# Kernel tuning notes

Hardware: AMD Instinct MI355X
Metric: run time of the kernel (lower is better)

## Reference

```python
import jax, jax.numpy as jnp
import numpy as np

B, L, D, H = 2, 2048, 1024, 16


def setup_inputs() -> dict:
    key = jax.random.key(0)
    ks = jax.random.split(key, 6)
    return {
        "x": jax.random.normal(ks[0], (B, L, D), dtype=jnp.float32),
        "w_qkv": jax.random.normal(ks[1], (3 * D, D), dtype=jnp.float32) * (D ** -0.5),
        "b_qkv": jax.random.normal(ks[2], (3 * D,), dtype=jnp.float32) * 0.02,
        "w_out": jax.random.normal(ks[3], (D, D), dtype=jnp.float32) * (D ** -0.5),
        "b_out": jax.random.normal(ks[4], (D,), dtype=jnp.float32) * 0.02,
        "lam": jnp.float32(0.5),
        "heads": H,
    }


def reference(x, w_qkv, b_qkv, w_out, b_out, lam, heads):
    b, l, d = x.shape
    dh = d // heads
    scale = d ** -0.5  # NOTE: module scales by d_model**-0.5, not head_dim**-0.5

    qkv = x @ w_qkv.T + b_qkv                      # [B, L, 3D]
    qkv = qkv.reshape(b, l, 3, heads, dh)
    qkv = jnp.transpose(qkv, (2, 0, 3, 1, 4))      # [3, B, H, L, dh]
    q, k, v = qkv[0], qkv[1], qkv[2]

    k_prev = jnp.roll(k, shift=1, axis=2)          # roll along sequence dim

    s_cur = jnp.einsum("bhqd,bhkd->bhqk", q, k) * scale
    s_prev = jnp.einsum("bhqd,bhkd->bhqk", q, k_prev) * scale

    a1 = jax.nn.softmax(s_cur, axis=-1)
    a2 = jax.nn.softmax(s_prev, axis=-1)
    diff = lam * (a1 - a2)                         # dropout = identity (eval)

    o = jnp.einsum("bhqk,bhkd->bhqd", diff, v)     # [B, H, L, dh]
    o = jnp.transpose(o, (0, 2, 1, 3)).reshape(b, l, d)
    return o @ w_out.T + b_out
```

## Files before the change

kernel.cpp:

```cpp
#include <hip/hip_runtime.h>
#include <hip/hip_bf16.h>
#include <stdint.h>


typedef __attribute__((ext_vector_type(8))) short s16x8;
typedef __attribute__((ext_vector_type(4))) short s16x4;
typedef __attribute__((ext_vector_type(4))) float f32x4;

__device__ __forceinline__ float bf2f(unsigned short u) {
    union { unsigned int i; float f; } x; x.i = ((unsigned int)u) << 16; return x.f;
}
__device__ __forceinline__ unsigned short f2bf(float f) {
    union { float f; unsigned int i; } x; x.f = f;
    unsigned int r = x.i + 0x7FFFu + ((x.i >> 16) & 1u);
    return (unsigned short)(r >> 16);
}

__device__ __forceinline__ f32x4 mfma16(s16x4 a, s16x4 b, f32x4 c) {
#if __has_builtin(__builtin_amdgcn_mfma_f32_16x16x16bf16_1k)
    return __builtin_amdgcn_mfma_f32_16x16x16bf16_1k(a, b, c, 0, 0, 0);
#else
    f32x4 d;
    asm volatile("v_mfma_f32_16x16x16_bf16 %0, %1, %2, %3\n\ts_nop 7\n\ts_nop 3"
                 : "=v"(d) : "v"(a), "v"(b), "v"(c));
    return d;
#endif
}

__device__ __forceinline__ void gload16(const void* g, void* l) {
    auto gp = reinterpret_cast<const __attribute__((address_space(1))) unsigned int*>(
        reinterpret_cast<uintptr_t>(g));
    auto lp = reinterpret_cast<__attribute__((address_space(3))) unsigned int*>(
        reinterpret_cast<uintptr_t>(l));
    __builtin_amdgcn_global_load_lds(gp, lp, 16, 0, 0);
}

__global__ __launch_bounds__(256) void cvt_all(
    const float* __restrict__ x, const float* __restrict__ wq,
    const float* __restrict__ wo,
    unsigned short* __restrict__ xb, unsigned short* __restrict__ wqb,
    unsigned short* __restrict__ wob)
{
    int i4 = blockIdx.x * 256 + threadIdx.x;
    const float* src; unsigned short* dst; int off;
    if (i4 < 1048576)            { src = x;  dst = xb;  off = i4; }
    else if (i4 < 1048576 + 786432) { src = wq; dst = wqb; off = i4 - 1048576; }
    else                         { src = wo; dst = wob; off = i4 - 1835008; }
    float4 v = ((const float4*)src)[off];
    ushort4 u;
    u.x = f2bf(v.x); u.y = f2bf(v.y); u.z = f2bf(v.z); u.w = f2bf(v.w);
    ((ushort4*)dst)[off] = u;
}

__global__ __launch_bounds__(256) void vd_transpose(
    const unsigned short* __restrict__ qkvb, unsigned short* __restrict__ vdt)
{
    __shared__ unsigned short T[64][72];
    const int tid = threadIdx.x;
    const int j0 = blockIdx.x * 64;
    const int bh = blockIdx.y, b = bh >> 4, h = bh & 15;
    const unsigned short* vb = qkvb + (size_t)b * 2048 * 3072 + 2048 + h * 64;

    int r = tid >> 2, cq = tid & 3;
    int j = j0 + r, jn = (j + 1) & 2047;
    const unsigned short* p0 = vb + (size_t)j  * 3072 + cq * 16;
    const unsigned short* p1 = vb + (size_t)jn * 3072 + cq * 16;
    s16x8 a0 = *(const s16x8*)p0, a1 = *(const s16x8*)(p0 + 8);
    s16x8 b0 = *(const s16x8*)p1, b1 = *(const s16x8*)(p1 + 8);
#pragma unroll
    for (int u = 0; u < 8; ++u)
        T[cq * 16 + u][r] = f2bf(bf2f((unsigned short)a0[u]) - bf2f((unsigned short)b0[u]));
#pragma unroll
    for (int u = 0; u < 8; ++u)
        T[cq * 16 + 8 + u][r] = f2bf(bf2f((unsigned short)a1[u]) - bf2f((unsigned short)b1[u]));
    __syncthreads();

    int row = tid >> 2, sc = tid & 3;
    s16x8 o0 = *(const s16x8*)&T[row][sc * 16];
    s16x8 o1 = *(const s16x8*)&T[row][sc * 16 + 8];
    unsigned short* dst = vdt + ((size_t)bh * 64 + row) * 2048 + j0 + sc * 16;
    *(s16x8*)dst = o0;
    *(s16x8*)(dst + 8) = o1;
}

template <int OUT_BF16, int BN>
__global__ __launch_bounds__(256) void gemm_nt_mfma(
    const unsigned short* __restrict__ A,
    const unsigned short* __restrict__ Bm,
    const float* __restrict__ bias,
    void* __restrict__ C,
    int M, int N, int K, int nscale, float smul)
{
    constexpr int NT = BN / 32;
    __shared__ unsigned short As[2][128][32];
    __shared__ unsigned short Bs[2][BN][32];

    const int tid = threadIdx.x;
    const int wave = tid >> 6, lane = tid & 63;
    const int quad = lane >> 4, ln = lane & 15;
    const int wm = (wave >> 1) * 64, wn = (wave & 1) * (NT * 16);
    const int m0 = blockIdx.y * 128, n0 = blockIdx.x * BN;
    const int rA = wave * 16 + (lane >> 2);
    const int gsl = lane & 3;

    f32x4 acc[4][NT];
#pragma unroll
    for (int mt = 0; mt < 4; ++mt)
#pragma unroll
        for (int nt = 0; nt < NT; ++nt) acc[mt][nt] = f32x4{0.f, 0.f, 0.f, 0.f};

    auto stage = [&](int p, int k0) {
#pragma unroll
        for (int q = 0; q < 2; ++q) {
            int row = q * 64 + rA;
            int kg = gsl ^ ((row >> 1) & 3);
            gload16(A + (size_t)(m0 + row) * K + k0 + kg * 8,
                    &As[p][q * 64 + wave * 16][0]);
            if (q * 64 < BN)
                gload16(Bm + (size_t)(n0 + row) * K + k0 + kg * 8,
                        &Bs[p][q * 64 + wave * 16][0]);
        }
    };

    stage(0, 0);
    __syncthreads();
    int p = 0;
    for (int k0 = 0; k0 < K; k0 += 32) {
        if (k0 + 32 < K) stage(p ^ 1, k0 + 32);
        s16x8 af[4], bfr[NT];
#pragma unroll
        for (int mt = 0; mt < 4; ++mt) {
            int rr = wm + mt * 16 + ln;
            af[mt] = *(const s16x8*)&As[p][rr][((quad ^ ((rr >> 1) & 3)) & 3) * 8];
        }
#pragma unroll
        for (int nt = 0; nt < NT; ++nt) {
            int rr = wn + nt * 16 + ln;
            bfr[nt] = *(const s16x8*)&Bs[p][rr][((quad ^ ((rr >> 1) & 3)) & 3) * 8];
        }
#pragma unroll
        for (int mt = 0; mt < 4; ++mt)
#pragma unroll
            for (int nt = 0; nt < NT; ++nt)
                acc[mt][nt] = __builtin_amdgcn_mfma_f32_16x16x32_bf16(
                    af[mt], bfr[nt], acc[mt][nt], 0, 0, 0);
        __syncthreads();
        p ^= 1;
    }

    float bb[NT];
#pragma unroll
    for (int nt = 0; nt < NT; ++nt) bb[nt] = bias[n0 + wn + nt * 16 + ln];
#pragma unroll
    for (int mt = 0; mt < 4; ++mt)
#pragma unroll
        for (int nt = 0; nt < NT; ++nt) {
            int col = n0 + wn + nt * 16 + ln;
            float sc = (col < nscale) ? smul : 1.f;
#pragma unroll
            for (int rg = 0; rg < 4; ++rg) {
                int row = m0 + wm + mt * 16 + quad * 4 + rg;
                float v = (acc[mt][nt][rg] + bb[nt]) * sc;
                if (OUT_BF16)
                    ((unsigned short*)C)[(size_t)row * N + col] = f2bf(v);
                else
                    ((float*)C)[(size_t)row * N + col] = v;
            }
        }
}

__global__ __launch_bounds__(256) void diff_attn_v5(
    const unsigned short* __restrict__ qkv,
    const unsigned short* __restrict__ vdt,
    const float* __restrict__ lam_p,
    unsigned short* __restrict__ o_ws)
{
    constexpr int L = 2048, TD = 3072;

    __shared__ unsigned short Ks[2][64][64];
    __shared__ unsigned short Vs[2][64][64];

    const int tid = threadIdx.x;
    const int wave = tid >> 6, lane = tid & 63;
    const int quad = lane >> 4, ln = lane & 15;
    const int bh = blockIdx.y, b = bh >> 4, h = bh & 15;
    const int q0 = blockIdx.x * 128;
    const size_t seqbase = (size_t)b * L;
    const unsigned short* base = qkv + seqbase * TD + h * 64;
    const unsigned short* kb = base + 1024;
    const unsigned short* vbase = vdt + (size_t)bh * 64 * 2048;

    const int lsl = lane >> 3;
    const int cgl = (lane & 7) ^ lsl;

    s16x8 qf[2][2];
#pragma unroll
    for (int s = 0; s < 2; ++s) {
        const unsigned short* qrow =
            base + (size_t)(q0 + wave * 32 + s * 16 + ln) * TD;
        qf[s][0] = *(const s16x8*)(qrow + quad * 8);
        qf[s][1] = *(const s16x8*)(qrow + 32 + quad * 8);
    }

    auto stage = [&](int p, int j0) {
        const unsigned short* k0p = kb + (size_t)(j0 + wave * 16 + lsl) * TD + cgl * 8;
        gload16(k0p,                  &Ks[p][wave * 16][0]);
        gload16(k0p + (size_t)8 * TD, &Ks[p][wave * 16 + 8][0]);
        const unsigned short* v0p = vbase + (size_t)(wave * 16 + lsl) * 2048 + j0 + cgl * 8;
        gload16(v0p,            &Vs[p][wave * 16][0]);
        gload16(v0p + 8 * 2048, &Vs[p][wave * 16 + 8][0]);
    };

    f32x4 Ot[2][4];
    f32x4 lacc[2];
#pragma unroll
    for (int s = 0; s < 2; ++s) {
        lacc[s] = f32x4{0.f, 0.f, 0.f, 0.f};
#pragma unroll
        for (int mt = 0; mt < 4; ++mt) Ot[s][mt] = f32x4{0.f, 0.f, 0.f, 0.f};
    }

    const s16x4 ones = {(short)0x3F80, (short)0x3F80, (short)0x3F80, (short)0x3F80};
    const int kx0 = (quad ^ (ln & 7)) << 3;
    const int kx1 = ((quad + 4) ^ (ln & 7)) << 3;

    stage(0, 0);
    __syncthreads();
    int p = 0;
    for (int kt = 0; kt < 32; ++kt) {
        if (kt + 1 < 32) stage(p ^ 1, (kt + 1) * 64);

        f32x4 ST[2][4];
#pragma unroll
        for (int t = 0; t < 4; ++t) {
            s16x8 k0 = *(const s16x8*)&Ks[p][t * 16 + ln][kx0];
            s16x8 k1 = *(const s16x8*)&Ks[p][t * 16 + ln][kx1];
#pragma unroll
            for (int s = 0; s < 2; ++s) {
                f32x4 z = f32x4{0.f, 0.f, 0.f, 0.f};
                z = __builtin_amdgcn_mfma_f32_16x16x32_bf16(k0, qf[s][0], z, 0, 0, 0);
                z = __builtin_amdgcn_mfma_f32_16x16x32_bf16(k1, qf[s][1], z, 0, 0, 0);
                ST[s][t] = z;
            }
        }

        s16x4 pf[2][4];
#pragma unroll
        for (int s = 0; s < 2; ++s)
#pragma unroll
            for (int t = 0; t < 4; ++t) {
                unsigned int b0 = __builtin_bit_cast(unsigned int,
                    __builtin_amdgcn_exp2f(ST[s][t][0]));
                unsigned int b1 = __builtin_bit_cast(unsigned int,
                    __builtin_amdgcn_exp2f(ST[s][t][1]));
                unsigned int b2 = __builtin_bit_cast(unsigned int,
                    __builtin_amdgcn_exp2f(ST[s][t][2]));
                unsigned int b3 = __builtin_bit_cast(unsigned int,
                    __builtin_amdgcn_exp2f(ST[s][t][3]));
                unsigned int lo = (b0 >> 16) | (b1 & 0xFFFF0000u);
                unsigned int hi = (b2 >> 16) | (b3 & 0xFFFF0000u);
                uint2 pk = make_uint2(lo, hi);
                pf[s][t] = __builtin_bit_cast(s16x4, pk);
            }

#pragma unroll
        for (int s = 0; s < 2; ++s)
#pragma unroll
            for (int t = 0; t < 4; ++t)
                lacc[s] = mfma16(ones, pf[s][t], lacc[s]);

#pragma unroll
        for (int t = 0; t < 4; ++t) {
#pragma unroll
            for (int mt = 0; mt < 4; ++mt) {
                int chunk = (2 * t + (quad >> 1)) ^ (ln & 7);
                s16x4 vf = *(const s16x4*)&Vs[p][mt * 16 + ln][chunk * 8 + (quad & 1) * 4];
#pragma unroll
                for (int s = 0; s < 2; ++s)
                    Ot[s][mt] = mfma16(vf, pf[s][t], Ot[s][mt]);
            }
        }
        __syncthreads();
        p ^= 1;
    }

    const float lam = lam_p[0];
#pragma unroll
    for (int s = 0; s < 2; ++s) {
        float inv = lam / lacc[s][0];
        int row = q0 + wave * 32 + s * 16 + ln;
        unsigned short* orow = o_ws + (seqbase + row) * 1024 + h * 64 + quad * 4;
#pragma unroll
        for (int mt = 0; mt < 4; ++mt) {
            ushort4 u;
            u.x = f2bf(Ot[s][mt][0] * inv);
            u.y = f2bf(Ot[s][mt][1] * inv);
            u.z = f2bf(Ot[s][mt][2] * inv);
            u.w = f2bf(Ot[s][mt][3] * inv);
            *(ushort4*)(orow + mt * 16) = u;
        }
    }
}

extern "C" void kernel_launch(void* const* d_in, const int* in_sizes, int n_in,
                              void* d_out, int out_size, void* d_ws, size_t ws_size,
                              hipStream_t stream) {
    const float* x     = (const float*)d_in[0];
    const float* w_qkv = (const float*)d_in[1];
    const float* b_qkv = (const float*)d_in[2];
    const float* w_out = (const float*)d_in[3];
    const float* b_out = (const float*)d_in[4];
    const float* lam   = (const float*)d_in[5];
    float* out = (float*)d_out;

    unsigned short* xb   = (unsigned short*)d_ws;
    unsigned short* wqb  = xb   + (size_t)4096 * 1024;
    unsigned short* wob  = wqb  + (size_t)3072 * 1024;
    unsigned short* qkvb = wob  + (size_t)1024 * 1024;
    unsigned short* ob   = qkvb + (size_t)4096 * 3072;
    unsigned short* vdt  = ob   + (size_t)4096 * 1024;

    cvt_all<<<8192, 256, 0, stream>>>(x, w_qkv, w_out, xb, wqb, wob);

    gemm_nt_mfma<1, 128><<<dim3(24, 32), 256, 0, stream>>>(
        xb, wqb, b_qkv, qkvb, 4096, 3072, 1024, 1024, 0.045084222f);

    vd_transpose<<<dim3(32, 32), 256, 0, stream>>>(qkvb, vdt);

    diff_attn_v5<<<dim3(16, 32), 256, 0, stream>>>(qkvb, vdt, lam, ob);

    gemm_nt_mfma<0, 64><<<dim3(16, 32), 256, 0, stream>>>(
        ob, wob, b_out, out, 4096, 1024, 1024, 0, 1.f);
}
```

Baseline: 198.6 us.

## Split key tiles across two wave groups in attention with shared-memory reduction

The attention kernel now runs 8 waves per block instead of 4. Each group of 4 waves handles half of every 64-key tile: two of the four 16-key sub-tiles for the score, exp and PV MFMAs. K/V staging is spread over all 8 waves, so each wave issues one load per tile instead of two. At the end, the second group writes its partial output and row-sum accumulators to LDS, and the first group adds them, normalises and stores. The goal is more waves in flight to hide latency with only 512 blocks on the device, at the cost of extra LDS, a final reduction barrier and lower MFMA work per wave between barriers.

Measured after the change: 189.2 us. -4.7%, faster.

```diff
diff --git a/kernel.cpp b/kernel.cpp
--- a/kernel.cpp
+++ b/kernel.cpp
@@ -169,7 +169,7 @@
         }
 }
 
-__global__ __launch_bounds__(256) void diff_attn_v5(
+__global__ __launch_bounds__(512) void diff_attn_v6(
     const unsigned short* __restrict__ qkv,
     const unsigned short* __restrict__ vdt,
     const float* __restrict__ lam_p,
@@ -179,9 +179,12 @@
 
     __shared__ unsigned short Ks[2][64][64];
     __shared__ unsigned short Vs[2][64][64];
+    __shared__ f32x4 Red[4][2][4][64];
+    __shared__ float Lred[4][2][64];
 
     const int tid = threadIdx.x;
     const int wave = tid >> 6, lane = tid & 63;
+    const int qw = wave & 3, jw = wave >> 2;
     const int quad = lane >> 4, ln = lane & 15;
     const int bh = blockIdx.y, b = bh >> 4, h = bh & 15;
     const int q0 = blockIdx.x * 128;
@@ -197,18 +200,16 @@
 #pragma unroll
     for (int s = 0; s < 2; ++s) {
         const unsigned short* qrow =
-            base + (size_t)(q0 + wave * 32 + s * 16 + ln) * TD;
+            base + (size_t)(q0 + qw * 32 + s * 16 + ln) * TD;
         qf[s][0] = *(const s16x8*)(qrow + quad * 8);
         qf[s][1] = *(const s16x8*)(qrow + 32 + quad * 8);
     }
 
     auto stage = [&](int p, int j0) {
-        const unsigned short* k0p = kb + (size_t)(j0 + wave * 16 + lsl) * TD + cgl * 8;
-        gload16(k0p,                  &Ks[p][wave * 16][0]);
-        gload16(k0p + (size_t)8 * TD, &Ks[p][wave * 16 + 8][0]);
-        const unsigned short* v0p = vbase + (size_t)(wave * 16 + lsl) * 2048 + j0 + cgl * 8;
-        gload16(v0p,            &Vs[p][wave * 16][0]);
-        gload16(v0p + 8 * 2048, &Vs[p][wave * 16 + 8][0]);
+        const unsigned short* k0p = kb + (size_t)(j0 + wave * 8 + lsl) * TD + cgl * 8;
+        gload16(k0p, &Ks[p][wave * 8][0]);
+        const unsigned short* v0p = vbase + (size_t)(wave * 8 + lsl) * 2048 + j0 + cgl * 8;
+        gload16(v0p, &Vs[p][wave * 8][0]);
     };
 
     f32x4 Ot[2][4];
@@ -230,11 +231,12 @@
     for (int kt = 0; kt < 32; ++kt) {
         if (kt + 1 < 32) stage(p ^ 1, (kt + 1) * 64);
 
-        f32x4 ST[2][4];
-#pragma unroll
-        for (int t = 0; t < 4; ++t) {
-            s16x8 k0 = *(const s16x8*)&Ks[p][t * 16 + ln][kx0];
-            s16x8 k1 = *(const s16x8*)&Ks[p][t * 16 + ln][kx1];
+        f32x4 ST[2][2];
+#pragma unroll
+        for (int t = 0; t < 2; ++t) {
+            const int t2 = jw * 2 + t;
+            s16x8 k0 = *(const s16x8*)&Ks[p][t2 * 16 + ln][kx0];
+            s16x8 k1 = *(const s16x8*)&Ks[p][t2 * 16 + ln][kx1];
 #pragma unroll
             for (int s = 0; s < 2; ++s) {
                 f32x4 z = f32x4{0.f, 0.f, 0.f, 0.f};
@@ -244,11 +246,11 @@
             }
         }
 
-        s16x4 pf[2][4];
+        s16x4 pf[2][2];
 #pragma unroll
         for (int s = 0; s < 2; ++s)
 #pragma unroll
-            for (int t = 0; t < 4; ++t) {
+            for (int t = 0; t < 2; ++t) {
                 unsigned int b0 = __builtin_bit_cast(unsigned int,
                     __builtin_amdgcn_exp2f(ST[s][t][0]));
                 unsigned int b1 = __builtin_bit_cast(unsigned int,
@@ -266,14 +268,15 @@
 #pragma unroll
         for (int s = 0; s < 2; ++s)
 #pragma unroll
-            for (int t = 0; t < 4; ++t)
+            for (int t = 0; t < 2; ++t)
                 lacc[s] = mfma16(ones, pf[s][t], lacc[s]);
 
 #pragma unroll
-        for (int t = 0; t < 4; ++t) {
+        for (int t = 0; t < 2; ++t) {
+            const int t2 = jw * 2 + t;
 #pragma unroll
             for (int mt = 0; mt < 4; ++mt) {
-                int chunk = (2 * t + (quad >> 1)) ^ (ln & 7);
+                int chunk = (2 * t2 + (quad >> 1)) ^ (ln & 7);
                 s16x4 vf = *(const s16x4*)&Vs[p][mt * 16 + ln][chunk * 8 + (quad & 1) * 4];
 #pragma unroll
                 for (int s = 0; s < 2; ++s)
@@ -284,20 +287,33 @@
         p ^= 1;
     }
 
-    const float lam = lam_p[0];
-#pragma unroll
-    for (int s = 0; s < 2; ++s) {
-        float inv = lam / lacc[s][0];
-        int row = q0 + wave * 32 + s * 16 + ln;
-        unsigned short* orow = o_ws + (seqbase + row) * 1024 + h * 64 + quad * 4;
-#pragma unroll
-        for (int mt = 0; mt < 4; ++mt) {
-            ushort4 u;
-            u.x = f2bf(Ot[s][mt][0] * inv);
-            u.y = f2bf(Ot[s][mt][1] * inv);
-            u.z = f2bf(Ot[s][mt][2] * inv);
-            u.w = f2bf(Ot[s][mt][3] * inv);
-            *(ushort4*)(orow + mt * 16) = u;
+    if (jw == 1) {
+#pragma unroll
+        for (int s = 0; s < 2; ++s) {
+            Lred[qw][s][lane] = lacc[s][0];
+#pragma unroll
+            for (int mt = 0; mt < 4; ++mt) Red[qw][s][mt][lane] = Ot[s][mt];
+        }
+    }
+    __syncthreads();
+    if (jw == 0) {
+        const float lam = lam_p[0];
+#pragma unroll
+        for (int s = 0; s < 2; ++s) {
+            float lsum = lacc[s][0] + Lred[qw][s][lane];
+            float inv = lam / lsum;
+            int row = q0 + qw * 32 + s * 16 + ln;
+            unsigned short* orow = o_ws + (seqbase + row) * 1024 + h * 64 + quad * 4;
+#pragma unroll
+            for (int mt = 0; mt < 4; ++mt) {
+                f32x4 r = Red[qw][s][mt][lane];
+                ushort4 u;
+                u.x = f2bf((Ot[s][mt][0] + r[0]) * inv);
+                u.y = f2bf((Ot[s][mt][1] + r[1]) * inv);
+                u.z = f2bf((Ot[s][mt][2] + r[2]) * inv);
+                u.w = f2bf((Ot[s][mt][3] + r[3]) * inv);
+                *(ushort4*)(orow + mt * 16) = u;
+            }
         }
     }
 }
@@ -327,7 +343,7 @@
 
     vd_transpose<<<dim3(32, 32), 256, 0, stream>>>(qkvb, vdt);
 
-    diff_attn_v5<<<dim3(16, 32), 256, 0, stream>>>(qkvb, vdt, lam, ob);
+    diff_attn_v6<<<dim3(16, 32), 512, 0, stream>>>(qkvb, vdt, lam, ob);
 
     gemm_nt_mfma<0, 64><<<dim3(16, 32), 256, 0, stream>>>(
         ob, wob, b_out, out, 4096, 1024, 1024, 0, 1.f);
```
